# Kernel tuning notes

Hardware: AMD Instinct MI355X
Metric: run time of the kernel (lower is better)

The kernel has to match this reference:

```python
import jax, jax.numpy as jnp
import numpy as np

ACTION_DIM = 32   # params['ACTION_DIM']
ITERATIONS = 4    # params['CEM_ITERATIONS']
CEM_BATCH = 64    # params['CEM_BATCH']
TOPK = 6          # params['CEM_TOPK']
STATE_DIM = 64
HIDDEN = 128
B_ENV = 8192


def _q_function(states, actions, W1, b1, W2, b2):
    # Q(s,a): 2-layer MLP on concat(state, action). states/actions: [CEM_BATCH, B_env, *]
    x = jnp.concatenate([states, actions], axis=-1)      # [CB, B_env, S+A]
    h = jax.nn.relu(x @ W1 + b1)                         # [CB, B_env, H]
    return (h @ W2 + b2)[..., 0]                         # [CB, B_env]


def setup_inputs() -> dict:
    key = jax.random.key(0)
    ks = jax.random.split(key, 3)
    state = jax.random.normal(ks[0], (B_ENV, STATE_DIM), dtype=jnp.float32)
    W1 = jax.random.normal(ks[1], (STATE_DIM + ACTION_DIM, HIDDEN), dtype=jnp.float32) * 0.05
    b1 = jnp.zeros((HIDDEN,), jnp.float32)
    W2 = jax.random.normal(ks[2], (HIDDEN, 1), dtype=jnp.float32) * 0.05
    b2 = jnp.zeros((1,), jnp.float32)
    return {"state": state, "W1": W1, "b1": b1, "W2": W2, "b2": b2}


def reference(state, W1, b1, W2, b2):
    B_env = state.shape[0]
    mean = jnp.zeros((B_env, ACTION_DIM), state.dtype)
    std = jnp.ones((B_env, ACTION_DIM), state.dtype)
    # states = torch.cat(batch * [state.unsqueeze(0)]) -> broadcast, no copy
    states = jnp.broadcast_to(state[None], (CEM_BATCH,) + state.shape)
    base_key = jax.random.key(42)
    best_action = None
    for i in range(ITERATIONS):
        eps = jax.random.normal(jax.random.fold_in(base_key, i),
                                (CEM_BATCH, B_env, ACTION_DIM), state.dtype)
        actions = mean[None] + std[None] * eps            # Normal(mean,std).sample((batch,))
        Qs = jax.lax.stop_gradient(_q_function(states, actions, W1, b1, W2, b2))  # no_grad
        # torch: Qs.topk(k, dim=0)[1] -> [TOPK, B_env]
        Is = jax.lax.top_k(Qs.T, TOPK)[1].T               # [TOPK, B_env]
        # faithful to torch zip(actions, Is): sel[j, e] = actions[j, Is[j, e]]
        sel = actions[jnp.arange(TOPK)[:, None], Is]      # [TOPK, B_env, A]
        mean = sel.mean(axis=0)
        std = sel.std(axis=0, ddof=1)                     # torch default unbiased std
        best_action = sel[0]
    return best_action
```

## Files before the change

kernel.cpp:

```cpp
#include <hip/hip_runtime.h>
#include <cstdint>


#define PARTW 0

#define TF_C 0x1BD11BDAu

__host__ __device__ __forceinline__ void tf20(uint32_t ks0, uint32_t ks1,
                                              uint32_t x0, uint32_t x1,
                                              uint32_t& o0, uint32_t& o1) {
  uint32_t ks2 = ks0 ^ ks1 ^ TF_C;
  x0 += ks0; x1 += ks1;
#define TF_RND(r) { x0 += x1; x1 = (x1 << (r)) | (x1 >> (32 - (r))); x1 ^= x0; }
  TF_RND(13) TF_RND(15) TF_RND(26) TF_RND(6)
  x0 += ks1; x1 += ks2 + 1u;
  TF_RND(17) TF_RND(29) TF_RND(16) TF_RND(24)
  x0 += ks2; x1 += ks0 + 2u;
  TF_RND(13) TF_RND(15) TF_RND(26) TF_RND(6)
  x0 += ks0; x1 += ks1 + 3u;
  TF_RND(17) TF_RND(29) TF_RND(16) TF_RND(24)
  x0 += ks1; x1 += ks2 + 4u;
  TF_RND(13) TF_RND(15) TF_RND(26) TF_RND(6)
  x0 += ks2; x1 += ks0 + 5u;
#undef TF_RND
  o0 = x0; o1 = x1;
}

__host__ __device__ __forceinline__ uint32_t pbits(uint32_t k0, uint32_t k1,
                                                   uint32_t f) {
  uint32_t o0, o1;
  tf20(k0, k1, 0u, f, o0, o1);
#if PARTW == 0
  return o0 ^ o1;
#elif PARTW == 1
  return o0;
#else
  return o1;
#endif
}

__device__ __forceinline__ float eps_from_bits(uint32_t bits) {
#pragma clang fp contract(off)
  const float LO = __uint_as_float(0xbf7fffffu);
  float f = __uint_as_float((bits >> 9) | 0x3f800000u) - 1.0f;
  float u = fmaxf(LO, f * 2.0f + LO);
  float t = -(u * u);
  float w_large = logf(t + 1.0f);
  float w_small = ((-0.5f * t) + 1.0f) * t;
  float w = (fabsf(t) < 1e-4f) ? w_small : w_large;
  w = -w;
  float p;
  if (w < 5.0f) {
    float ww = w - 2.5f;
    p = 2.81022636e-08f;
    p = 3.43273939e-07f + p * ww;
    p = -3.5233877e-06f + p * ww;
    p = -4.39150654e-06f + p * ww;
    p = 0.00021858087f + p * ww;
    p = -0.00125372503f + p * ww;
    p = -0.00417768164f + p * ww;
    p = 0.246640727f + p * ww;
    p = 1.50140941f + p * ww;
  } else {
    float ww = sqrtf(w) - 3.0f;
    p = -0.000200214257f;
    p = 0.000100950558f + p * ww;
    p = 0.00134934322f + p * ww;
    p = -0.00367342844f + p * ww;
    p = 0.00573950773f + p * ww;
    p = -0.0076224613f + p * ww;
    p = 0.00943887047f + p * ww;
    p = 1.00167406f + p * ww;
    p = 2.83297682f + p * ww;
  }
  float r = p * u;
  return __uint_as_float(0x3fb504f3u) * r;
}

__device__ __forceinline__ void gen_eps(uint32_t k0, uint32_t k1, int env,
                                        int lane, float eps[32]) {
  const uint32_t base = (uint32_t)lane * 262144u + (uint32_t)env * 32u;
#pragma unroll
  for (int k = 0; k < 32; ++k)
    eps[k] = eps_from_bits(pbits(k0, k1, base + (uint32_t)k));
}

__device__ __forceinline__ float qeval(const float* __restrict__ Srow,
                                       const float* __restrict__ W1aT,
                                       const float* __restrict__ b1,
                                       const float* __restrict__ W2,
                                       float b2v, const float a[32]) {
  float q = 0.0f;
#pragma unroll 4
  for (int j = 0; j < 128; ++j) {
    float h = Srow[j];
    const float* wr = W1aT + j * 32;
#pragma unroll
    for (int k = 0; k < 32; ++k) h = __builtin_fmaf(a[k], wr[k], h);
    h = h + b1[j];
    h = fmaxf(h, 0.0f);
    q = __builtin_fmaf(h, W2[j], q);
  }
  return q + b2v;
}

__device__ __forceinline__ void top6(float q, int lane, int top[6]) {
  float qv = q;
#pragma unroll
  for (int i = 0; i < 6; ++i) {
    float v = qv;
    int idx = lane;
#pragma unroll
    for (int off = 1; off < 64; off <<= 1) {
      float ov = __shfl_xor(v, off, 64);
      int oi = __shfl_xor(idx, off, 64);
      if (ov > v || (ov == v && oi < idx)) { v = ov; idx = oi; }
    }
    top[i] = __builtin_amdgcn_readfirstlane(idx);
    if (lane == idx) qv = -__builtin_inff();
  }
}

__device__ __forceinline__ void stats6(const float sel[6], float& mean, float& sd) {
#pragma clang fp contract(off)
  float s = ((((sel[0] + sel[1]) + sel[2]) + sel[3]) + sel[4]) + sel[5];
  mean = s / 6.0f;
  float d0 = sel[0] - mean, d1 = sel[1] - mean, d2 = sel[2] - mean;
  float d3 = sel[3] - mean, d4 = sel[4] - mean, d5 = sel[5] - mean;
  float p0 = d0 * d0, p1 = d1 * d1, p2 = d2 * d2;
  float p3 = d3 * d3, p4 = d4 * d4, p5 = d5 * d5;
  float ss = ((((p0 + p1) + p2) + p3) + p4) + p5;
  sd = sqrtf(ss / 5.0f);
}

__device__ __forceinline__ float rdlane(float v, int l) {
  return __int_as_float(__builtin_amdgcn_readlane(__float_as_int(v), l));
}

__global__ void __launch_bounds__(128) k_prep_spre(const float* __restrict__ state,
                                                   const float* __restrict__ W1,
                                                   float* __restrict__ S_pre) {
  const int b = blockIdx.x;
  const int j = threadIdx.x;
  float h = 0.0f;
  const float* srow = state + (size_t)b * 64;
#pragma unroll 8
  for (int k = 0; k < 64; ++k) h = __builtin_fmaf(srow[k], W1[k * 128 + j], h);
  S_pre[(size_t)b * 128 + j] = h;
}

__global__ void __launch_bounds__(256) k_prep_misc(const float* __restrict__ W1,
                                                   float* __restrict__ W1aT,
                                                   float* __restrict__ T0,
                                                   float* __restrict__ meanW,
                                                   float* __restrict__ stdW,
                                                   uint32_t K0, uint32_t K1) {
  const int tid = blockIdx.x * 256 + threadIdx.x;
  if (tid < 4096) {
    int j = tid >> 5, k = tid & 31;
    W1aT[tid] = W1[(64 + k) * 128 + j];
  }
  {
    int i = tid >> 11, rem = tid & 2047;
    uint32_t f = (uint32_t)i * 262144u + (uint32_t)rem;
    T0[tid] = eps_from_bits(pbits(K0, K1, f));
  }
  if (tid < 2048) { meanW[tid] = 0.0f; stdW[tid] = 1.0f; }
}

__global__ void __launch_bounds__(256) k_stage1(const float* __restrict__ S_pre,
    const float* __restrict__ W1aT, const float* __restrict__ b1,
    const float* __restrict__ W2, const float* __restrict__ b2,
    const float* __restrict__ Tcur, float* __restrict__ Tnext,
    float* __restrict__ meanW, float* __restrict__ stdW, uint32_t K0,
    uint32_t K1, uint32_t NK0, uint32_t NK1) {
  const int lane = threadIdx.x & 63;
  const int e = __builtin_amdgcn_readfirstlane((int)(blockIdx.x * 4 + (threadIdx.x >> 6)));
  const int kk = lane & 31;
  float eps[32];
  gen_eps(K0, K1, e, lane, eps);
  float a[32];
  {
#pragma clang fp contract(off)
#pragma unroll
    for (int k = 0; k < 32; ++k) {
      float mk = meanW[e * 32 + k];
      float sk = stdW[e * 32 + k];
      a[k] = mk + sk * eps[k];
    }
  }
  float q = qeval(S_pre + (size_t)e * 128, W1aT, b1, W2, b2[0], a);
  int top[6];
  top6(q, lane, top);
  float sel[6];
#pragma unroll
  for (int i = 0; i < 6; ++i) sel[i] = Tcur[(size_t)((i * 64 + top[i]) * 32) + kk];
  float vmean, vsd;
  stats6(sel, vmean, vsd);
  if (lane < 32) {
    meanW[e * 32 + kk] = vmean;
    stdW[e * 32 + kk] = vsd;
  }
#pragma unroll
  for (int t = 0; t < 3; ++t) {
    int m = lane * 3 + t;
    int i = m >> 5, k = m & 31;
    uint32_t f = (uint32_t)i * 262144u + (uint32_t)e * 32u + (uint32_t)k;
    float ev = eps_from_bits(pbits(NK0, NK1, f));
    float mk = __shfl(vmean, k, 64);
    float sk = __shfl(vsd, k, 64);
    float val;
    {
#pragma clang fp contract(off)
      val = mk + sk * ev;
    }
    Tnext[(size_t)((i * 64 + e) * 32 + k)] = val;
  }
}

__global__ void __launch_bounds__(256) k_main(const float* __restrict__ S_pre,
    const float* __restrict__ W1aT, const float* __restrict__ b1,
    const float* __restrict__ W2, const float* __restrict__ b2,
    const float* __restrict__ T, float* __restrict__ out, uint4 kx, uint4 ky) {
  const int lane = threadIdx.x & 63;
  const int b = __builtin_amdgcn_readfirstlane((int)(blockIdx.x * 4 + (threadIdx.x >> 6)));
  const float* Srow = S_pre + (size_t)b * 128;
  const float bb2 = b2[0];
  const int kk = lane & 31;
  float vmean = 0.0f, vsd = 1.0f;
  for (int it = 0; it < 4; ++it) {
    uint32_t K0 = it == 0 ? kx.x : it == 1 ? kx.y : it == 2 ? kx.z : kx.w;
    uint32_t K1 = it == 0 ? ky.x : it == 1 ? ky.y : it == 2 ? ky.z : ky.w;
    float eps[32];
    gen_eps(K0, K1, b, lane, eps);
    float a[32];
    if (it == 0) {
#pragma unroll
      for (int k = 0; k < 32; ++k) a[k] = eps[k];
    } else {
#pragma clang fp contract(off)
#pragma unroll
      for (int k = 0; k < 32; ++k) {
        float mk = rdlane(vmean, k);
        float sk = rdlane(vsd, k);
        a[k] = mk + sk * eps[k];
      }
    }
    float q = qeval(Srow, W1aT, b1, W2, bb2, a);
    int top[6];
    top6(q, lane, top);
    const float* Tt = T + it * 12288;
    float sel0 = Tt[(size_t)(top[0] * 32) + kk];
    if (it == 3) {
      if (lane < 32) out[(size_t)b * 32 + kk] = sel0;
    } else {
      float sel[6];
      sel[0] = sel0;
#pragma unroll
      for (int i = 1; i < 6; ++i) sel[i] = Tt[(size_t)((i * 64 + top[i]) * 32) + kk];
      stats6(sel, vmean, vsd);
    }
  }
}

extern "C" void kernel_launch(void* const* d_in, const int* in_sizes, int n_in,
                              void* d_out, int out_size, void* d_ws,
                              size_t ws_size, hipStream_t stream) {
  const float* state = (const float*)d_in[0];
  const float* W1 = (const float*)d_in[1];
  const float* b1 = (const float*)d_in[2];
  const float* W2 = (const float*)d_in[3];
  const float* b2 = (const float*)d_in[4];
  float* out = (float*)d_out;

  float* ws = (float*)d_ws;
  float* S_pre = ws;
  float* W1aT = ws + 1048576;
  float* T = W1aT + 4096;
  float* meanW = T + 4 * 12288;
  float* stdW = meanW + 2048;

  uint32_t K0[4], K1[4];
  for (uint32_t i = 0; i < 4; ++i) {
    uint32_t a, bb;
    tf20(0u, 42u, 0u, i, a, bb);
    K0[i] = a;
    K1[i] = bb;
  }

  k_prep_spre<<<8192, 128, 0, stream>>>(state, W1, S_pre);
  k_prep_misc<<<48, 256, 0, stream>>>(W1, W1aT, T, meanW, stdW, K0[0], K1[0]);
  for (int it = 0; it < 3; ++it)
    k_stage1<<<16, 256, 0, stream>>>(S_pre, W1aT, b1, W2, b2, T + it * 12288,
                                     T + (it + 1) * 12288, meanW, stdW, K0[it],
                                     K1[it], K0[it + 1], K1[it + 1]);
  k_main<<<2048, 256, 0, stream>>>(S_pre, W1aT, b1, W2, b2, T, out,
                                   make_uint4(K0[0], K0[1], K0[2], K0[3]),
                                   make_uint4(K1[0], K1[1], K1[2], K1[3]));
}
```

Baseline: 583.5 us.

## Process two environments per wavefront in main CEM kernel to share weight loads

Each wavefront now handles two environments, evaluating both Q-networks in one loop so each W1aT/b1/W2 load feeds two FMA chains. Per-lane mean/std are split so lanes 0-31 serve environment A and lanes 32-63 serve B, and the grid is halved. This aims to raise arithmetic per weight load and reuse eps generation overhead, at the cost of more registers (two 32-float action arrays) and fewer waves in flight.

```diff
diff --git a/kernel.cpp b/kernel.cpp
--- a/kernel.cpp
+++ b/kernel.cpp
@@ -1,8 +1,6 @@
 #include <hip/hip_runtime.h>
 #include <cstdint>
 
-
-#define PARTW 0
 
 #define TF_C 0x1BD11BDAu
 
@@ -30,13 +28,7 @@
                                                    uint32_t f) {
   uint32_t o0, o1;
   tf20(k0, k1, 0u, f, o0, o1);
-#if PARTW == 0
   return o0 ^ o1;
-#elif PARTW == 1
-  return o0;
-#else
-  return o1;
-#endif
 }
 
 __device__ __forceinline__ float eps_from_bits(uint32_t bits) {
@@ -104,6 +96,37 @@
   return q + b2v;
 }
 
+__device__ __forceinline__ void qeval2(const float* __restrict__ SrowA,
+                                       const float* __restrict__ SrowB,
+                                       const float* __restrict__ W1aT,
+                                       const float* __restrict__ b1,
+                                       const float* __restrict__ W2,
+                                       float b2v, const float aA[32],
+                                       const float aB[32], float& qAo,
+                                       float& qBo) {
+  float qA = 0.0f, qB = 0.0f;
+#pragma unroll 4
+  for (int j = 0; j < 128; ++j) {
+    float h0 = SrowA[j];
+    float h1 = SrowB[j];
+    const float* wr = W1aT + j * 32;
+#pragma unroll
+    for (int k = 0; k < 32; ++k) {
+      float w = wr[k];
+      h0 = __builtin_fmaf(aA[k], w, h0);
+      h1 = __builtin_fmaf(aB[k], w, h1);
+    }
+    float bj = b1[j];
+    h0 = fmaxf(h0 + bj, 0.0f);
+    h1 = fmaxf(h1 + bj, 0.0f);
+    float wj = W2[j];
+    qA = __builtin_fmaf(h0, wj, qA);
+    qB = __builtin_fmaf(h1, wj, qB);
+  }
+  qAo = qA + b2v;
+  qBo = qB + b2v;
+}
+
 __device__ __forceinline__ void top6(float q, int lane, int top[6]) {
   float qv = q;
 #pragma unroll
@@ -223,41 +246,48 @@
     const float* __restrict__ W2, const float* __restrict__ b2,
     const float* __restrict__ T, float* __restrict__ out, uint4 kx, uint4 ky) {
   const int lane = threadIdx.x & 63;
-  const int b = __builtin_amdgcn_readfirstlane((int)(blockIdx.x * 4 + (threadIdx.x >> 6)));
-  const float* Srow = S_pre + (size_t)b * 128;
+  const int g = __builtin_amdgcn_readfirstlane((int)(blockIdx.x * 4 + (threadIdx.x >> 6)));
+  const int bA = 2 * g, bB = 2 * g + 1;
+  const float* SrowA = S_pre + (size_t)bA * 128;
+  const float* SrowB = S_pre + (size_t)bB * 128;
   const float bb2 = b2[0];
   const int kk = lane & 31;
   float vmean = 0.0f, vsd = 1.0f;
   for (int it = 0; it < 4; ++it) {
     uint32_t K0 = it == 0 ? kx.x : it == 1 ? kx.y : it == 2 ? kx.z : kx.w;
     uint32_t K1 = it == 0 ? ky.x : it == 1 ? ky.y : it == 2 ? ky.z : ky.w;
-    float eps[32];
-    gen_eps(K0, K1, b, lane, eps);
-    float a[32];
-    if (it == 0) {
-#pragma unroll
-      for (int k = 0; k < 32; ++k) a[k] = eps[k];
-    } else {
+    float aA[32], aB[32];
+    gen_eps(K0, K1, bA, lane, aA);
+    gen_eps(K0, K1, bB, lane, aB);
+    if (it != 0) {
 #pragma clang fp contract(off)
 #pragma unroll
       for (int k = 0; k < 32; ++k) {
-        float mk = rdlane(vmean, k);
-        float sk = rdlane(vsd, k);
-        a[k] = mk + sk * eps[k];
+        float mkA = rdlane(vmean, k), skA = rdlane(vsd, k);
+        float mkB = rdlane(vmean, 32 + k), skB = rdlane(vsd, 32 + k);
+        aA[k] = mkA + skA * aA[k];
+        aB[k] = mkB + skB * aB[k];
       }
     }
-    float q = qeval(Srow, W1aT, b1, W2, bb2, a);
-    int top[6];
-    top6(q, lane, top);
+    float qA, qB;
+    qeval2(SrowA, SrowB, W1aT, b1, W2, bb2, aA, aB, qA, qB);
+    int topA[6], topB[6];
+    top6(qA, lane, topA);
+    top6(qB, lane, topB);
     const float* Tt = T + it * 12288;
-    float sel0 = Tt[(size_t)(top[0] * 32) + kk];
+    int t0 = lane < 32 ? topA[0] : topB[0];
+    float sel0 = Tt[(size_t)(t0 * 32) + kk];
     if (it == 3) {
-      if (lane < 32) out[(size_t)b * 32 + kk] = sel0;
+      int env = lane < 32 ? bA : bB;
+      out[(size_t)env * 32 + kk] = sel0;
     } else {
       float sel[6];
       sel[0] = sel0;
 #pragma unroll
-      for (int i = 1; i < 6; ++i) sel[i] = Tt[(size_t)((i * 64 + top[i]) * 32) + kk];
+      for (int i = 1; i < 6; ++i) {
+        int ti = lane < 32 ? topA[i] : topB[i];
+        sel[i] = Tt[(size_t)((i * 64 + ti) * 32) + kk];
+      }
       stats6(sel, vmean, vsd);
     }
   }
@@ -294,7 +324,7 @@
     k_stage1<<<16, 256, 0, stream>>>(S_pre, W1aT, b1, W2, b2, T + it * 12288,
                                      T + (it + 1) * 12288, meanW, stdW, K0[it],
                                      K1[it], K0[it + 1], K1[it + 1]);
-  k_main<<<2048, 256, 0, stream>>>(S_pre, W1aT, b1, W2, b2, T, out,
+  k_main<<<1024, 256, 0, stream>>>(S_pre, W1aT, b1, W2, b2, T, out,
                                    make_uint4(K0[0], K0[1], K0[2], K0[3]),
                                    make_uint4(K1[0], K1[1], K1[2], K1[3]));
 }
```

Result: slower. 648.9 us (+11.2%).

## Split fused CEM loop into per-iteration eps generation and Q-eval kernels

Applied to the files above, without the earlier changes.

Noise generation moves out of the monolithic main kernel into a separate wide kernel that writes a 64 MB eps buffer each iteration. A per-iteration main kernel then reads eps, applies the mean and std stored in global memory, evaluates Q, and writes the new stats. The prep kernels are merged into one launch. This trades the register-heavy inline Threefry and erfinv work for large global memory traffic and more launches, and the old fused path is kept as a fallback when the workspace is too small.

```diff
diff --git a/kernel.cpp b/kernel.cpp
--- a/kernel.cpp
+++ b/kernel.cpp
@@ -1,8 +1,6 @@
 #include <hip/hip_runtime.h>
 #include <cstdint>
 
-
-#define PARTW 0
 
 #define TF_C 0x1BD11BDAu
 
@@ -30,13 +28,7 @@
                                                    uint32_t f) {
   uint32_t o0, o1;
   tf20(k0, k1, 0u, f, o0, o1);
-#if PARTW == 0
   return o0 ^ o1;
-#elif PARTW == 1
-  return o0;
-#else
-  return o1;
-#endif
 }
 
 __device__ __forceinline__ float eps_from_bits(uint32_t bits) {
@@ -137,35 +129,32 @@
   return __int_as_float(__builtin_amdgcn_readlane(__float_as_int(v), l));
 }
 
-__global__ void __launch_bounds__(128) k_prep_spre(const float* __restrict__ state,
-                                                   const float* __restrict__ W1,
-                                                   float* __restrict__ S_pre) {
-  const int b = blockIdx.x;
-  const int j = threadIdx.x;
-  float h = 0.0f;
-  const float* srow = state + (size_t)b * 64;
+__global__ void __launch_bounds__(128) k_prep(const float* __restrict__ state,
+    const float* __restrict__ W1, float* __restrict__ S_pre,
+    float* __restrict__ W1aT, float* __restrict__ T0,
+    float* __restrict__ s1mean, float* __restrict__ s1std, uint32_t K0,
+    uint32_t K1) {
+  const int bid = blockIdx.x;
+  if (bid < 8192) {
+    const int j = threadIdx.x;
+    float h = 0.0f;
+    const float* srow = state + (size_t)bid * 64;
 #pragma unroll 8
-  for (int k = 0; k < 64; ++k) h = __builtin_fmaf(srow[k], W1[k * 128 + j], h);
-  S_pre[(size_t)b * 128 + j] = h;
-}
-
-__global__ void __launch_bounds__(256) k_prep_misc(const float* __restrict__ W1,
-                                                   float* __restrict__ W1aT,
-                                                   float* __restrict__ T0,
-                                                   float* __restrict__ meanW,
-                                                   float* __restrict__ stdW,
-                                                   uint32_t K0, uint32_t K1) {
-  const int tid = blockIdx.x * 256 + threadIdx.x;
-  if (tid < 4096) {
-    int j = tid >> 5, k = tid & 31;
-    W1aT[tid] = W1[(64 + k) * 128 + j];
-  }
-  {
-    int i = tid >> 11, rem = tid & 2047;
-    uint32_t f = (uint32_t)i * 262144u + (uint32_t)rem;
-    T0[tid] = eps_from_bits(pbits(K0, K1, f));
-  }
-  if (tid < 2048) { meanW[tid] = 0.0f; stdW[tid] = 1.0f; }
+    for (int k = 0; k < 64; ++k) h = __builtin_fmaf(srow[k], W1[k * 128 + j], h);
+    S_pre[(size_t)bid * 128 + j] = h;
+  } else {
+    const int tid = (bid - 8192) * 128 + threadIdx.x;
+    if (tid < 4096) {
+      int j = tid >> 5, k = tid & 31;
+      W1aT[tid] = W1[(64 + k) * 128 + j];
+    }
+    {
+      int i = tid >> 11, rem = tid & 2047;
+      uint32_t f = (uint32_t)i * 262144u + (uint32_t)rem;
+      T0[tid] = eps_from_bits(pbits(K0, K1, f));
+    }
+    if (tid < 2048) { s1mean[tid] = 0.0f; s1std[tid] = 1.0f; }
+  }
 }
 
 __global__ void __launch_bounds__(256) k_stage1(const float* __restrict__ S_pre,
@@ -218,6 +207,62 @@
   }
 }
 
+__global__ void __launch_bounds__(256) k_eps(float* __restrict__ ebuf,
+                                             uint32_t K0, uint32_t K1) {
+  const int env = blockIdx.x;
+  const int c = threadIdx.x & 63;
+  const int w = threadIdx.x >> 6;
+  const uint32_t base = (uint32_t)c * 262144u + (uint32_t)env * 32u;
+  float* dst = ebuf + (size_t)env * 2048 + c;
+#pragma unroll
+  for (int r = 0; r < 8; ++r) {
+    int k = w * 8 + r;
+    dst[(size_t)k * 64] = eps_from_bits(pbits(K0, K1, base + (uint32_t)k));
+  }
+}
+
+__global__ void __launch_bounds__(256) k_main_it(const float* __restrict__ S_pre,
+    const float* __restrict__ W1aT, const float* __restrict__ b1,
+    const float* __restrict__ W2, const float* __restrict__ b2,
+    const float* __restrict__ Tt, const float* __restrict__ ebuf,
+    float* __restrict__ mMean, float* __restrict__ mStd,
+    float* __restrict__ out, int is_first, int is_last) {
+  const int lane = threadIdx.x & 63;
+  const int b = __builtin_amdgcn_readfirstlane((int)(blockIdx.x * 4 + (threadIdx.x >> 6)));
+  const int kk = lane & 31;
+  const float* esrc = ebuf + (size_t)b * 2048 + lane;
+  float a[32];
+#pragma unroll
+  for (int k = 0; k < 32; ++k) a[k] = esrc[(size_t)k * 64];
+  if (!is_first) {
+#pragma clang fp contract(off)
+#pragma unroll
+    for (int k = 0; k < 32; ++k) {
+      float mk = mMean[b * 32 + k];
+      float sk = mStd[b * 32 + k];
+      a[k] = mk + sk * a[k];
+    }
+  }
+  float q = qeval(S_pre + (size_t)b * 128, W1aT, b1, W2, b2[0], a);
+  int top[6];
+  top6(q, lane, top);
+  float sel0 = Tt[(size_t)(top[0] * 32) + kk];
+  if (is_last) {
+    if (lane < 32) out[(size_t)b * 32 + kk] = sel0;
+  } else {
+    float sel[6];
+    sel[0] = sel0;
+#pragma unroll
+    for (int i = 1; i < 6; ++i) sel[i] = Tt[(size_t)((i * 64 + top[i]) * 32) + kk];
+    float vmean, vsd;
+    stats6(sel, vmean, vsd);
+    if (lane < 32) {
+      mMean[b * 32 + kk] = vmean;
+      mStd[b * 32 + kk] = vsd;
+    }
+  }
+}
+
 __global__ void __launch_bounds__(256) k_main(const float* __restrict__ S_pre,
     const float* __restrict__ W1aT, const float* __restrict__ b1,
     const float* __restrict__ W2, const float* __restrict__ b2,
@@ -231,19 +276,15 @@
   for (int it = 0; it < 4; ++it) {
     uint32_t K0 = it == 0 ? kx.x : it == 1 ? kx.y : it == 2 ? kx.z : kx.w;
     uint32_t K1 = it == 0 ? ky.x : it == 1 ? ky.y : it == 2 ? ky.z : ky.w;
-    float eps[32];
-    gen_eps(K0, K1, b, lane, eps);
     float a[32];
-    if (it == 0) {
-#pragma unroll
-      for (int k = 0; k < 32; ++k) a[k] = eps[k];
-    } else {
+    gen_eps(K0, K1, b, lane, a);
+    if (it != 0) {
 #pragma clang fp contract(off)
 #pragma unroll
       for (int k = 0; k < 32; ++k) {
         float mk = rdlane(vmean, k);
         float sk = rdlane(vsd, k);
-        a[k] = mk + sk * eps[k];
+        a[k] = mk + sk * a[k];
       }
     }
     float q = qeval(Srow, W1aT, b1, W2, bb2, a);
@@ -275,10 +316,15 @@
 
   float* ws = (float*)d_ws;
   float* S_pre = ws;
-  float* W1aT = ws + 1048576;
+  float* W1aT = S_pre + 1048576;
   float* T = W1aT + 4096;
-  float* meanW = T + 4 * 12288;
-  float* stdW = meanW + 2048;
+  float* s1mean = T + 4 * 12288;
+  float* s1std = s1mean + 2048;
+  float* mMean = s1std + 2048;
+  float* mStd = mMean + 262144;
+  float* ebuf = mStd + 262144;
+  const size_t need_split = (size_t)(1048576 + 4096 + 4 * 12288 + 2048 + 2048 +
+                                     262144 + 262144 + 16777216) * 4;
 
   uint32_t K0[4], K1[4];
   for (uint32_t i = 0; i < 4; ++i) {
@@ -288,13 +334,28 @@
     K1[i] = bb;
   }
 
-  k_prep_spre<<<8192, 128, 0, stream>>>(state, W1, S_pre);
-  k_prep_misc<<<48, 256, 0, stream>>>(W1, W1aT, T, meanW, stdW, K0[0], K1[0]);
-  for (int it = 0; it < 3; ++it)
-    k_stage1<<<16, 256, 0, stream>>>(S_pre, W1aT, b1, W2, b2, T + it * 12288,
-                                     T + (it + 1) * 12288, meanW, stdW, K0[it],
-                                     K1[it], K0[it + 1], K1[it + 1]);
-  k_main<<<2048, 256, 0, stream>>>(S_pre, W1aT, b1, W2, b2, T, out,
-                                   make_uint4(K0[0], K0[1], K0[2], K0[3]),
-                                   make_uint4(K1[0], K1[1], K1[2], K1[3]));
-}
+  k_prep<<<8288, 128, 0, stream>>>(state, W1, S_pre, W1aT, T, s1mean, s1std,
+                                   K0[0], K1[0]);
+  if (ws_size >= need_split) {
+    for (int it = 0; it < 4; ++it) {
+      k_eps<<<8192, 256, 0, stream>>>(ebuf, K0[it], K1[it]);
+      if (it < 3)
+        k_stage1<<<16, 256, 0, stream>>>(S_pre, W1aT, b1, W2, b2,
+                                         T + it * 12288, T + (it + 1) * 12288,
+                                         s1mean, s1std, K0[it], K1[it],
+                                         K0[it + 1], K1[it + 1]);
+      k_main_it<<<2048, 256, 0, stream>>>(S_pre, W1aT, b1, W2, b2,
+                                          T + it * 12288, ebuf, mMean, mStd,
+                                          out, it == 0 ? 1 : 0,
+                                          it == 3 ? 1 : 0);
+    }
+  } else {
+    for (int it = 0; it < 3; ++it)
+      k_stage1<<<16, 256, 0, stream>>>(S_pre, W1aT, b1, W2, b2, T + it * 12288,
+                                       T + (it + 1) * 12288, s1mean, s1std,
+                                       K0[it], K1[it], K0[it + 1], K1[it + 1]);
+    k_main<<<2048, 256, 0, stream>>>(S_pre, W1aT, b1, W2, b2, T, out,
+                                     make_uint4(K0[0], K0[1], K0[2], K0[3]),
+                                     make_uint4(K1[0], K1[1], K1[2], K1[3]));
+  }
+}
```

Measured after the change: 734.6 us. +25.9%, slower.
